# Performance work log

Measured on AMD Instinct MI355X. Metric: run time of the kernel, lower is better.

## Reference

```python
import jax, jax.numpy as jnp
import numpy as np

M, K, N, G = 4096, 4096, 4096, 128


def setup_inputs() -> dict:
    key = jax.random.key(0)
    k1, k2, k3 = jax.random.split(key, 3)
    a = jax.random.normal(k1, (M, K), dtype=jnp.float16)
    # 4-bit unsigned quantized weights, values in [0, 16)
    w_q = jax.random.randint(k2, (K, N), 0, 16, dtype=jnp.int32)
    # group-wise scales: one per (k-group, n); small magnitude keeps fp16 output in range
    scale = jax.random.uniform(k3, (K // G, N), dtype=jnp.float16, minval=0.001, maxval=0.02)
    return {"a": a, "w_q": w_q, "scale": scale, "group_size": G}


def reference(a, w_q, scale, group_size):
    # Dequantize: w[k, n] = w_q[k, n] * scale[k // group_size, n]
    scale_full = jnp.repeat(scale, group_size, axis=0)  # [K, N]
    w = w_q.astype(a.dtype) * scale_full                # fp16 dequantized weight
    out = jnp.matmul(a, w, preferred_element_type=jnp.float32)
    return out.astype(jnp.float16)
```

## Files before the change

### kernel.cpp

```cpp
#include <hip/hip_runtime.h>
#include <hip/hip_fp16.h>

#define MDIM 4096
#define NDIM 4096
#define KDIM 4096
#define NT 256
#define WBLK 4096

typedef _Float16 f16x8 __attribute__((ext_vector_type(8)));
typedef float f32x4 __attribute__((ext_vector_type(4)));
typedef unsigned int u32;
typedef unsigned short u16;

__device__ inline __half2 as_half2(u32 u) { return __builtin_bit_cast(__half2, u); }
__device__ inline u32 as_u32(__half2 h) { return __builtin_bit_cast(u32, h); }
__device__ inline u32 pkrtz(float a, float b) {
  return __builtin_bit_cast(u32, __builtin_amdgcn_cvt_pkrtz(a, b));
}

__device__ inline void load16_to_lds(const void* g, void* l) {
  __builtin_amdgcn_global_load_lds(
      (__attribute__((address_space(1))) const u32*)g,
      (__attribute__((address_space(3))) u32*)l,
      16, 0, 0);
}

template <int VM>
__device__ __forceinline__ void wait_vmcnt() {
  if constexpr (VM == 8)
    asm volatile("s_waitcnt vmcnt(8)" ::: "memory");
  else if constexpr (VM == 4)
    asm volatile("s_waitcnt vmcnt(4)" ::: "memory");
  else
    asm volatile("s_waitcnt vmcnt(0)" ::: "memory");
}

__global__ __launch_bounds__(NT) void prep(const float* __restrict__ A,
                                           _Float16* __restrict__ A16,
                                           const int* __restrict__ Wq,
                                           const float* __restrict__ Sc,
                                           _Float16* __restrict__ Wt) {
  __shared__ u32 Lt[64 * 33];
  const int tid = threadIdx.x;

  if (blockIdx.x >= WBLK) {
    const size_t b = blockIdx.x - WBLK;
    const size_t base = (b * NT + tid) * 8;
    const float4 f0 = *(const float4*)(A + base);
    const float4 f1 = *(const float4*)(A + base + 4);
    u32 pk[4];
    pk[0] = pkrtz(f0.x, f0.y);
    pk[1] = pkrtz(f0.z, f0.w);
    pk[2] = pkrtz(f1.x, f1.y);
    pk[3] = pkrtz(f1.z, f1.w);
    *(uint4*)(A16 + base) = *(const uint4*)pk;
    return;
  }

  const int n0 = (blockIdx.x & 63) * 64;
  const int k0 = (blockIdx.x >> 6) * 64;
  const int g = k0 >> 7;

#pragma unroll
  for (int r = 0; r < 2; ++r) {
    const int idx = r * 256 + tid;
    const int kp = idx >> 4;
    const int col4 = (idx & 15) * 4;
    const int4 va = *(const int4*)(Wq + (size_t)(k0 + 2 * kp) * NDIM + n0 + col4);
    const int4 vb = *(const int4*)(Wq + (size_t)(k0 + 2 * kp + 1) * NDIM + n0 + col4);
    const float4 s = *(const float4*)(Sc + (size_t)g * NDIM + n0 + col4);
    const float sf[4] = {s.x, s.y, s.z, s.w};
    const int av[4] = {va.x, va.y, va.z, va.w};
    const int bv[4] = {vb.x, vb.y, vb.z, vb.w};
#pragma unroll
    for (int i = 0; i < 4; ++i) {
      const __half hs = __float2half(sf[i]);
      const __half2 s2 = __half2half2(hs);
      const __half2 nb = __half2half2(__hmul(hs, __float2half(-1024.0f)));
      const u32 u = (u32)av[i] | ((u32)bv[i] << 16) | 0x64006400u;
      Lt[(size_t)(col4 + i) * 33 + kp] = as_u32(__hfma2(as_half2(u), s2, nb));
    }
  }
  __syncthreads();

#pragma unroll
  for (int r = 0; r < 2; ++r) {
    const int idx = r * 256 + tid;
    const int n = idx >> 3;
    const int k2c = (idx & 7) * 4;
    u32 v[4];
#pragma unroll
    for (int j = 0; j < 4; ++j) v[j] = Lt[(size_t)n * 33 + k2c + j];
    *(uint4*)(Wt + (size_t)(n0 + n) * KDIM + k0 + k2c * 2) = *(const uint4*)v;
  }
}

__global__ __launch_bounds__(512, 2) void gemm_f16(const _Float16* __restrict__ A16,
                                                   const _Float16* __restrict__ Wt,
                                                   float* __restrict__ C) {
  __shared__ __align__(16) _Float16 As[4 * 256 * 32];
  __shared__ __align__(16) _Float16 Bs[4 * 256 * 32];

  const int tid = threadIdx.x;
  const int bx = blockIdx.x & 15;
  const int by = blockIdx.x >> 4;
  const int m_base = by * 256;
  const int n_base = bx * 256;

  const int wave = tid >> 6;
  const int lane = tid & 63;
  const int l15 = lane & 15;
  const int quad = lane >> 4;
  const int mq = wave >> 2;
  const int nq = wave & 3;
  const int gq = (l15 >> 1) & 3;
  const int pchunk = quad ^ gq;

  f32x4 acc[8][4];
#pragma unroll
  for (int i = 0; i < 8; ++i)
#pragma unroll
    for (int j = 0; j < 4; ++j) acc[i][j] = (f32x4)0.0f;

  auto stage = [&](int p) {
    const int T = p >> 1;
    const int h = p & 1;
    const int s = p & 3;
    const size_t kof = (size_t)T * 64 + (size_t)h * 32;
#pragma unroll
    for (int L = 0; L < 2; ++L) {
      const int cc = L * 512 + tid;
      const int row = cc >> 2;
      const int lch = (cc & 3) ^ ((row >> 1) & 3);
      load16_to_lds(A16 + (size_t)(m_base + row) * KDIM + kof + lch * 8,
                    (char*)As + (size_t)s * 16384 + (size_t)cc * 16);
    }
#pragma unroll
    for (int L = 0; L < 2; ++L) {
      const int cc = L * 512 + tid;
      const int row = cc >> 2;
      const int lch = (cc & 3) ^ ((row >> 1) & 3);
      load16_to_lds(Wt + (size_t)(n_base + row) * KDIM + kof + lch * 8,
                    (char*)Bs + (size_t)s * 16384 + (size_t)cc * 16);
    }
  };

  auto phase_body = [&](int p, bool dostage) {
    __builtin_amdgcn_s_barrier();
    asm volatile("" ::: "memory");
    const int s = p & 3;
    const _Float16* Ab = (const _Float16*)((const char*)As + (size_t)s * 16384);
    const _Float16* Bb = (const _Float16*)((const char*)Bs + (size_t)s * 16384);
    f16x8 af[8], bf[4];
#pragma unroll
    for (int i = 0; i < 8; ++i) {
      const int row = mq * 128 + i * 16 + l15;
      af[i] = *(const f16x8*)(Ab + (size_t)row * 32 + pchunk * 8);
    }
#pragma unroll
    for (int j = 0; j < 4; ++j) {
      const int row = nq * 64 + j * 16 + l15;
      bf[j] = *(const f16x8*)(Bb + (size_t)row * 32 + pchunk * 8);
    }
    if (dostage) stage(p + 3);
    asm volatile("s_waitcnt lgkmcnt(0)" ::: "memory");
    __builtin_amdgcn_sched_barrier(0);
    __builtin_amdgcn_s_setprio(1);
#pragma unroll
    for (int i = 0; i < 8; ++i)
#pragma unroll
      for (int j = 0; j < 4; ++j)
        acc[i][j] = __builtin_amdgcn_mfma_f32_16x16x32_f16(af[i], bf[j],
                                                           acc[i][j], 0, 0, 0);
    __builtin_amdgcn_s_setprio(0);
  };

  stage(0);
  stage(1);
  stage(2);

  for (int p = 0; p < 125; ++p) {
    wait_vmcnt<8>();
    phase_body(p, true);
  }
  wait_vmcnt<8>();
  phase_body(125, false);
  wait_vmcnt<4>();
  phase_body(126, false);
  wait_vmcnt<0>();
  phase_body(127, false);

#pragma unroll
  for (int i = 0; i < 8; ++i) {
#pragma unroll
    for (int j = 0; j < 4; ++j) {
      const int col = n_base + nq * 64 + j * 16 + l15;
#pragma unroll
      for (int r = 0; r < 4; ++r) {
        const int row = m_base + mq * 128 + i * 16 + quad * 4 + r;
        C[(size_t)row * NDIM + col] = __half2float(__float2half(acc[i][j][r]));
      }
    }
  }
}

#define STR 72
__global__ __launch_bounds__(NT) void qgemm_fused(
    const float* __restrict__ A, const int* __restrict__ Wq,
    const float* __restrict__ Sc, float* __restrict__ C) {
  __shared__ __align__(16) _Float16 As[128 * STR];
  __shared__ __align__(16) _Float16 Bs[128 * STR];
  const int tid = threadIdx.x;
  const int bx = blockIdx.x & 31, by = blockIdx.x >> 5;
  const int m_base = by * 128, n_base = bx * 128;
  const int wave = tid >> 6, lane = tid & 63;
  const int l15 = lane & 15, quad = lane >> 4;
  const int wm = (wave & 1) * 64, wn = (wave >> 1) * 64;
  const int bn_local = tid & 127, bk_half = (tid >> 7) * 8;
  const int gn = n_base + bn_local;
  f32x4 acc[4][4];
#pragma unroll
  for (int i = 0; i < 4; ++i)
#pragma unroll
    for (int j = 0; j < 4; ++j) acc[i][j] = (f32x4)0.0f;
  for (int kt = 0; kt < KDIM / 64; ++kt) {
    const int k0 = kt * 64;
    __syncthreads();
#pragma unroll
    for (int i = 0; i < 8; ++i) {
      const int c = i * 256 + tid;
      const int row = c >> 4, col4 = (c & 15) * 4;
      const float4 f = *(const float4*)(A + (size_t)(m_base + row) * KDIM + k0 + col4);
      u32 pk[2];
      pk[0] = pkrtz(f.x, f.y);
      pk[1] = pkrtz(f.z, f.w);
      *(uint2*)&As[(size_t)row * STR + col4] = *(const uint2*)pk;
    }
    {
      const __half hs = __float2half(Sc[(size_t)(k0 >> 7) * NDIM + gn]);
      const __half2 s2 = __half2half2(hs);
      const __half2 nb2 = __half2half2(__hmul(hs, __float2half(-1024.0f)));
#pragma unroll
      for (int it = 0; it < 4; ++it) {
        const int k = bk_half + it * 16;
        u32 v[8];
#pragma unroll
        for (int j = 0; j < 8; ++j)
          v[j] = (u32)Wq[(size_t)(k0 + k + j) * NDIM + gn];
        u32 pk[4];
#pragma unroll
        for (int p = 0; p < 4; ++p) {
          u32 u = v[2 * p] | (v[2 * p + 1] << 16) | 0x64006400u;
          pk[p] = as_u32(__hfma2(as_half2(u), s2, nb2));
        }
        *(uint4*)&Bs[(size_t)bn_local * STR + k] = *(const uint4*)pk;
      }
    }
    __syncthreads();
#pragma unroll
    for (int ks = 0; ks < 64; ks += 32) {
      f16x8 af[4], bf[4];
#pragma unroll
      for (int i = 0; i < 4; ++i)
        af[i] = *(const f16x8*)&As[(size_t)(wm + i * 16 + l15) * STR + ks + quad * 8];
#pragma unroll
      for (int j = 0; j < 4; ++j)
        bf[j] = *(const f16x8*)&Bs[(size_t)(wn + j * 16 + l15) * STR + ks + quad * 8];
#pragma unroll
      for (int i = 0; i < 4; ++i)
#pragma unroll
        for (int j = 0; j < 4; ++j)
          acc[i][j] = __builtin_amdgcn_mfma_f32_16x16x32_f16(af[i], bf[j],
                                                             acc[i][j], 0, 0, 0);
    }
  }
#pragma unroll
  for (int i = 0; i < 4; ++i)
#pragma unroll
    for (int j = 0; j < 4; ++j) {
      const int col = n_base + wn + j * 16 + l15;
#pragma unroll
      for (int r = 0; r < 4; ++r) {
        const int row = m_base + wm + i * 16 + quad * 4 + r;
        C[(size_t)row * NDIM + col] = __half2float(__float2half(acc[i][j][r]));
      }
    }
}

extern "C" void kernel_launch(void* const* d_in, const int* in_sizes, int n_in,
                              void* d_out, int out_size, void* d_ws, size_t ws_size,
                              hipStream_t stream) {
  const float* a = (const float*)d_in[0];
  const int* wq = (const int*)d_in[1];
  const float* sc = (const float*)d_in[2];
  float* out = (float*)d_out;

  const size_t a16_bytes = (size_t)MDIM * KDIM * 2;
  const size_t wt_bytes = (size_t)NDIM * KDIM * 2;

  if (ws_size >= a16_bytes + wt_bytes) {
    _Float16* a16 = (_Float16*)d_ws;
    _Float16* wt = (_Float16*)((char*)d_ws + a16_bytes);
    const int a_blocks = (MDIM * KDIM) / (NT * 8);
    prep<<<WBLK + a_blocks, NT, 0, stream>>>(a, a16, wq, sc, wt);
    gemm_f16<<<(MDIM / 256) * (NDIM / 256), 512, 0, stream>>>(a16, wt, out);
  } else {
    qgemm_fused<<<(MDIM / 128) * (NDIM / 128), NT, 0, stream>>>(a, wq, sc, out);
  }
}
```

Measured before the change: 286.0 us.

## Merge prep and GEMM kernels into one persistent kernel with grid barrier

Replaces the separate dequant/convert prep kernel and the GEMM kernel with a single 256-block kernel. Each block first dequantizes and transposes its share of the weights and converts its share of A to fp16, then all blocks meet at a global atomic-counter barrier before running the GEMM. This aims to remove one kernel launch and its tail, but it adds a memset and a spin barrier. The barrier relies on all 256 blocks of 512 threads being resident at the same time; if they are not, the kernel deadlocks. The prep phase also now runs with fewer blocks and a serial 16-iteration loop per block.

```diff
diff --git a/kernel.cpp b/kernel.cpp
--- a/kernel.cpp
+++ b/kernel.cpp
@@ -5,7 +5,6 @@
 #define NDIM 4096
 #define KDIM 4096
 #define NT 256
-#define WBLK 4096
 
 typedef _Float16 f16x8 __attribute__((ext_vector_type(8)));
 typedef float f32x4 __attribute__((ext_vector_type(4)));
@@ -35,17 +34,60 @@
     asm volatile("s_waitcnt vmcnt(0)" ::: "memory");
 }
 
-__global__ __launch_bounds__(NT) void prep(const float* __restrict__ A,
-                                           _Float16* __restrict__ A16,
-                                           const int* __restrict__ Wq,
-                                           const float* __restrict__ Sc,
-                                           _Float16* __restrict__ Wt) {
+__global__ __launch_bounds__(512) void fused_all(const float* __restrict__ A,
+                                                 const int* __restrict__ Wq,
+                                                 const float* __restrict__ Sc,
+                                                 float* __restrict__ C,
+                                                 _Float16* __restrict__ A16,
+                                                 _Float16* __restrict__ Wt,
+                                                 u32* __restrict__ cnt) {
+  __shared__ __align__(16) _Float16 As[4 * 256 * 32];
+  __shared__ __align__(16) _Float16 Bs[4 * 256 * 32];
   __shared__ u32 Lt[64 * 33];
+
   const int tid = threadIdx.x;
-
-  if (blockIdx.x >= WBLK) {
-    const size_t b = blockIdx.x - WBLK;
-    const size_t base = (b * NT + tid) * 8;
+  const int b = blockIdx.x;
+
+  for (int i = 0; i < 16; ++i) {
+    const int w = b * 16 + i;
+    const int n0 = (w & 63) * 64;
+    const int k0 = (w >> 6) * 64;
+    const int g = k0 >> 7;
+
+    {
+      const int kp = tid >> 4;
+      const int col4 = (tid & 15) * 4;
+      const int4 va = *(const int4*)(Wq + (size_t)(k0 + 2 * kp) * NDIM + n0 + col4);
+      const int4 vb = *(const int4*)(Wq + (size_t)(k0 + 2 * kp + 1) * NDIM + n0 + col4);
+      const float4 s = *(const float4*)(Sc + (size_t)g * NDIM + n0 + col4);
+      const float sf[4] = {s.x, s.y, s.z, s.w};
+      const int av[4] = {va.x, va.y, va.z, va.w};
+      const int bv[4] = {vb.x, vb.y, vb.z, vb.w};
+#pragma unroll
+      for (int q = 0; q < 4; ++q) {
+        const __half hs = __float2half(sf[q]);
+        const __half2 s2 = __half2half2(hs);
+        const __half2 nb = __half2half2(__hmul(hs, __float2half(-1024.0f)));
+        const u32 u = (u32)av[q] | ((u32)bv[q] << 16) | 0x64006400u;
+        Lt[(size_t)(col4 + q) * 33 + kp] = as_u32(__hfma2(as_half2(u), s2, nb));
+      }
+    }
+    __syncthreads();
+    {
+      const int n = tid >> 3;
+      const int k2c = (tid & 7) * 4;
+      u32 v[4];
+#pragma unroll
+      for (int j = 0; j < 4; ++j) v[j] = Lt[(size_t)n * 33 + k2c + j];
+      *(uint4*)(Wt + (size_t)(n0 + n) * KDIM + k0 + k2c * 2) = *(const uint4*)v;
+    }
+    __syncthreads();
+  }
+
+#pragma unroll
+  for (int it = 0; it < 16; ++it) {
+    const size_t idx = (size_t)it * 131072 + (size_t)b * 512 + tid;
+    const size_t base = idx * 8;
     const float4 f0 = *(const float4*)(A + base);
     const float4 f1 = *(const float4*)(A + base + 4);
     u32 pk[4];
@@ -54,56 +96,19 @@
     pk[2] = pkrtz(f1.x, f1.y);
     pk[3] = pkrtz(f1.z, f1.w);
     *(uint4*)(A16 + base) = *(const uint4*)pk;
-    return;
-  }
-
-  const int n0 = (blockIdx.x & 63) * 64;
-  const int k0 = (blockIdx.x >> 6) * 64;
-  const int g = k0 >> 7;
-
-#pragma unroll
-  for (int r = 0; r < 2; ++r) {
-    const int idx = r * 256 + tid;
-    const int kp = idx >> 4;
-    const int col4 = (idx & 15) * 4;
-    const int4 va = *(const int4*)(Wq + (size_t)(k0 + 2 * kp) * NDIM + n0 + col4);
-    const int4 vb = *(const int4*)(Wq + (size_t)(k0 + 2 * kp + 1) * NDIM + n0 + col4);
-    const float4 s = *(const float4*)(Sc + (size_t)g * NDIM + n0 + col4);
-    const float sf[4] = {s.x, s.y, s.z, s.w};
-    const int av[4] = {va.x, va.y, va.z, va.w};
-    const int bv[4] = {vb.x, vb.y, vb.z, vb.w};
-#pragma unroll
-    for (int i = 0; i < 4; ++i) {
-      const __half hs = __float2half(sf[i]);
-      const __half2 s2 = __half2half2(hs);
-      const __half2 nb = __half2half2(__hmul(hs, __float2half(-1024.0f)));
-      const u32 u = (u32)av[i] | ((u32)bv[i] << 16) | 0x64006400u;
-      Lt[(size_t)(col4 + i) * 33 + kp] = as_u32(__hfma2(as_half2(u), s2, nb));
-    }
-  }
+  }
+
   __syncthreads();
-
-#pragma unroll
-  for (int r = 0; r < 2; ++r) {
-    const int idx = r * 256 + tid;
-    const int n = idx >> 3;
-    const int k2c = (idx & 7) * 4;
-    u32 v[4];
-#pragma unroll
-    for (int j = 0; j < 4; ++j) v[j] = Lt[(size_t)n * 33 + k2c + j];
-    *(uint4*)(Wt + (size_t)(n0 + n) * KDIM + k0 + k2c * 2) = *(const uint4*)v;
-  }
-}
-
-__global__ __launch_bounds__(512, 2) void gemm_f16(const _Float16* __restrict__ A16,
-                                                   const _Float16* __restrict__ Wt,
-                                                   float* __restrict__ C) {
-  __shared__ __align__(16) _Float16 As[4 * 256 * 32];
-  __shared__ __align__(16) _Float16 Bs[4 * 256 * 32];
-
-  const int tid = threadIdx.x;
-  const int bx = blockIdx.x & 15;
-  const int by = blockIdx.x >> 4;
+  if (tid == 0) {
+    __threadfence();
+    atomicAdd(cnt, 1u);
+    while (atomicAdd(cnt, 0u) < 256u) __builtin_amdgcn_s_sleep(2);
+    __threadfence();
+  }
+  __syncthreads();
+
+  const int bx = b & 15;
+  const int by = b >> 4;
   const int m_base = by * 256;
   const int n_base = bx * 256;
 
@@ -298,12 +303,12 @@
   const size_t a16_bytes = (size_t)MDIM * KDIM * 2;
   const size_t wt_bytes = (size_t)NDIM * KDIM * 2;
 
-  if (ws_size >= a16_bytes + wt_bytes) {
+  if (ws_size >= a16_bytes + wt_bytes + 4096) {
     _Float16* a16 = (_Float16*)d_ws;
     _Float16* wt = (_Float16*)((char*)d_ws + a16_bytes);
-    const int a_blocks = (MDIM * KDIM) / (NT * 8);
-    prep<<<WBLK + a_blocks, NT, 0, stream>>>(a, a16, wq, sc, wt);
-    gemm_f16<<<(MDIM / 256) * (NDIM / 256), 512, 0, stream>>>(a16, wt, out);
+    u32* cnt = (u32*)((char*)d_ws + a16_bytes + wt_bytes);
+    hipMemsetAsync(cnt, 0, 4, stream);
+    fused_all<<<256, 512, 0, stream>>>(a, wq, sc, out, a16, wt, cnt);
   } else {
     qgemm_fused<<<(MDIM / 128) * (NDIM / 128), NT, 0, stream>>>(a, wq, sc, out);
   }
```

After: 321.7 us. +12.5%, slower.
